# Optimization experiments

Hardware: AMD Instinct MI355X
Metric: run time of the kernel (lower is better)

## Reference

```python
import jax, jax.numpy as jnp
import numpy as np

N_QUBITS = 12
RANK = 1024
K = 4            # outcomes per qubit
D = 2 ** N_QUBITS
N_IDX = 1_000_000


def setup_inputs() -> dict:
    key = jax.random.key(0)
    k1, k2, k3, k4 = jax.random.split(key, 4)
    params = jax.random.normal(k1, (2, D, RANK), dtype=jnp.float32)
    M_real = jax.random.normal(k2, (K, 2, 2), dtype=jnp.float32)
    M_imag = jax.random.normal(k3, (K, 2, 2), dtype=jnp.float32)
    P_idxs = jax.random.randint(k4, (N_IDX,), 0, K ** N_QUBITS, dtype=jnp.int64)
    return {"params": params, "M_real": M_real, "M_imag": M_imag, "P_idxs": P_idxs}


def _qmt(rho, M, n_qubits):
    """Born rule: P[s1..sN] = Tr[(M_{s1} x ... x M_{sN}) rho].
    Sequential per-qubit contraction; T has shape [K^n, 2^(N-n), 2^(N-n)]."""
    T = rho[None, :, :]  # axes: (done outcomes, row legs j, col legs i)
    for _ in range(n_qubits):
        k, r, c = T.shape[0], T.shape[1] // 2, T.shape[2] // 2
        Tt = T.reshape(k, 2, r, 2, c)  # (k, j_n, j_rest, i_n, i_rest)
        # Tr contribution: sum_{i,j} M[s,i,j] * rho[j,i]
        T = jnp.einsum('sij,kjait->ksat', M, Tt).reshape(k * M.shape[0], r, c)
    return T.reshape(-1)  # [K^N] complex


def reference(params, M_real, M_imag, P_idxs):
    # rho = U U^H / Tr(U U^H)
    U = jax.lax.complex(params[0], params[1])            # [D, RANK] complex64
    rho = U @ U.conj().T                                  # [D, D]
    rho = rho / jnp.trace(rho)
    M = jax.lax.complex(M_real, M_imag)                   # [K, 2, 2] complex64
    P_all = _qmt(rho, M, N_QUBITS).real                   # [K^N] float32
    return P_all[P_idxs]
```

## Files before the change

### kernel.cpp

```cpp
#include <hip/hip_runtime.h>

#define D 4096
#define RANK 1024
#define UELEMS 4194304ULL
#define NTOT 16777216ULL
#define QSCALE 16000.0f

typedef __attribute__((ext_vector_type(4))) int i32x4;

__device__ float g_inv_tr[1];
__device__ float g_scale[D];
__device__ float g_mdre[16];
__device__ float g_mdim[16];

static __device__ __forceinline__ void load_lds16(const void* g, void* l) {
    __builtin_amdgcn_global_load_lds(
        (const __attribute__((address_space(1))) unsigned int*)g,
        (__attribute__((address_space(3))) unsigned int*)l, 16, 0, 0);
}

#define MFMA_I8 __builtin_amdgcn_mfma_i32_16x16x64_i8

__global__ __launch_bounds__(256) void convert_w_i8(const float* __restrict__ P,
                                                    const float* __restrict__ Mre,
                                                    const float* __restrict__ Mim,
                                                    char* __restrict__ Wh,
                                                    char* __restrict__ Wl)
{
    if (blockIdx.x == 0 && threadIdx.x < 16) {
        const int s = threadIdx.x >> 2, i = (threadIdx.x >> 1) & 1, j = threadIdx.x & 1;
        g_mdre[threadIdx.x] =  Mre[s * 4 + j * 2 + i];
        g_mdim[threadIdx.x] = -Mim[s * 4 + j * 2 + i];
    }

    const int w = threadIdx.x >> 6, lane = threadIdx.x & 63;
    const int row = blockIdx.x * 4 + w;

    float ur[16], ui[16];
    const float* pr = P + (size_t)row * RANK + lane * 16;
    const float* pi = P + UELEMS + (size_t)row * RANK + lane * 16;
    #pragma unroll
    for (int q = 0; q < 4; ++q) {
        const float4 a = ((const float4*)pr)[q];
        const float4 b = ((const float4*)pi)[q];
        ur[q * 4 + 0] = a.x; ur[q * 4 + 1] = a.y; ur[q * 4 + 2] = a.z; ur[q * 4 + 3] = a.w;
        ui[q * 4 + 0] = b.x; ui[q * 4 + 1] = b.y; ui[q * 4 + 2] = b.z; ui[q * 4 + 3] = b.w;
    }
    float mx = 0.f;
    #pragma unroll
    for (int e = 0; e < 16; ++e)
        mx = fmaxf(mx, fmaxf(fabsf(ur[e]), fabsf(ui[e])));
    #pragma unroll
    for (int off = 1; off < 64; off <<= 1)
        mx = fmaxf(mx, __shfl_xor(mx, off));
    const float inv = mx > 0.f ? QSCALE / mx : 0.f;
    if (lane == 0) g_scale[row] = mx / QSCALE;

    int hr[16], lr[16], hi[16], li[16];
    #pragma unroll
    for (int e = 0; e < 16; ++e) {
        float q = ur[e] * inv;
        float hf = rintf(q * 0.0078125f);
        hr[e] = (int)hf; lr[e] = (int)rintf(q - 128.f * hf);
        q = ui[e] * inv;
        hf = rintf(q * 0.0078125f);
        hi[e] = (int)hf; li[e] = (int)rintf(q - 128.f * hf);
    }
    uint4 phr, plr, phi, pli;
    unsigned* dst[4] = {(unsigned*)&phr, (unsigned*)&plr, (unsigned*)&phi, (unsigned*)&pli};
    #pragma unroll
    for (int q = 0; q < 4; ++q) {
        unsigned a = 0, b = 0, c = 0, d = 0;
        #pragma unroll
        for (int k = 0; k < 4; ++k) {
            const int sh = k * 8;
            a |= (unsigned)(hr[q * 4 + k] & 255) << sh;
            b |= (unsigned)(lr[q * 4 + k] & 255) << sh;
            c |= (unsigned)(hi[q * 4 + k] & 255) << sh;
            d |= (unsigned)(li[q * 4 + k] & 255) << sh;
        }
        dst[0][q] = a; dst[1][q] = b; dst[2][q] = c; dst[3][q] = d;
    }
    const size_t b1 = (size_t)row * 2048 + lane * 16;
    *(uint4*)&Wh[b1] = phr;          *(uint4*)&Wl[b1] = plr;
    *(uint4*)&Wh[b1 + 1024] = phi;   *(uint4*)&Wl[b1 + 1024] = pli;
}

__global__ __launch_bounds__(256, 2) void gemm_rho_i8(const char* __restrict__ Wh,
                                                      const char* __restrict__ Wl,
                                                      float2* __restrict__ rho)
{
    __shared__ __align__(16) char sA[2][4][64 * 64];
    __shared__ __align__(16) char sB[2][4][64 * 64];

    const int g = blockIdx.x;
    int bi = (int)((sqrtf(8.f * (float)g + 1.f) - 1.f) * 0.5f);
    while (bi * (bi + 1) / 2 > g) --bi;
    while ((bi + 1) * (bi + 2) / 2 <= g) ++bi;
    const int bj = g - bi * (bi + 1) / 2;
    const int row0 = bi << 6, col0 = bj << 6;

    const int t = threadIdx.x;
    const int lane = t & 63, w = t >> 6;
    const int wr = w >> 1, wc = w & 1;

    const int ra = t >> 2;
    const int kca = (t & 3) ^ ((ra >> 1) & 3);
    const size_t aoff = (size_t)(row0 + ra) * 2048 + kca * 16;
    const size_t boff = (size_t)(col0 + ra) * 2048 + kca * 16;
    const int ldso = t * 16;

    const int m = lane & 15, gq = lane >> 4;
    const int fko = (gq ^ ((m >> 1) & 3)) * 16;

    i32x4 rehh[2][2], remx[2][2], iphh[2][2], ipmx[2][2], iqhh[2][2], iqmx[2][2];
    #pragma unroll
    for (int i = 0; i < 2; ++i)
        #pragma unroll
        for (int j = 0; j < 2; ++j) {
            rehh[i][j] = (i32x4){0, 0, 0, 0}; remx[i][j] = (i32x4){0, 0, 0, 0};
            iphh[i][j] = (i32x4){0, 0, 0, 0}; ipmx[i][j] = (i32x4){0, 0, 0, 0};
            iqhh[i][j] = (i32x4){0, 0, 0, 0}; iqmx[i][j] = (i32x4){0, 0, 0, 0};
        }

    char* const sA0 = &sA[0][0][0];
    char* const sB0 = &sB[0][0][0];

    load_lds16(Wh + aoff,        sA0 + ldso);
    load_lds16(Wl + aoff,        sA0 + 4096  + ldso);
    load_lds16(Wh + aoff + 1024, sA0 + 8192  + ldso);
    load_lds16(Wl + aoff + 1024, sA0 + 12288 + ldso);
    load_lds16(Wh + boff,        sB0 + ldso);
    load_lds16(Wl + boff,        sB0 + 4096  + ldso);
    load_lds16(Wh + boff + 1024, sB0 + 8192  + ldso);
    load_lds16(Wl + boff + 1024, sB0 + 12288 + ldso);
    __syncthreads();

#define DO_MFMA_J(j)                                                          \
    _Pragma("unroll")                                                         \
    for (int i = 0; i < 2; ++i) {                                             \
        i32x4 r;                                                              \
        r = rehh[i][j];                                                       \
        r = MFMA_I8(fa1h[i], b1h[j], r, 0, 0, 0);                             \
        r = MFMA_I8(fa2h[i], b2h[j], r, 0, 0, 0);                             \
        rehh[i][j] = r;                                                       \
        r = remx[i][j];                                                       \
        r = MFMA_I8(fa1h[i], b1l[j], r, 0, 0, 0);                             \
        r = MFMA_I8(fa1l[i], b1h[j], r, 0, 0, 0);                             \
        r = MFMA_I8(fa2h[i], b2l[j], r, 0, 0, 0);                             \
        r = MFMA_I8(fa2l[i], b2h[j], r, 0, 0, 0);                             \
        remx[i][j] = r;                                                       \
        r = MFMA_I8(fa2h[i], b1h[j], iphh[i][j], 0, 0, 0); iphh[i][j] = r;    \
        r = ipmx[i][j];                                                       \
        r = MFMA_I8(fa2h[i], b1l[j], r, 0, 0, 0);                             \
        r = MFMA_I8(fa2l[i], b1h[j], r, 0, 0, 0);                             \
        ipmx[i][j] = r;                                                       \
        r = MFMA_I8(fa1h[i], b2h[j], iqhh[i][j], 0, 0, 0); iqhh[i][j] = r;    \
        r = iqmx[i][j];                                                       \
        r = MFMA_I8(fa1h[i], b2l[j], r, 0, 0, 0);                             \
        r = MFMA_I8(fa1l[i], b2h[j], r, 0, 0, 0);                             \
        iqmx[i][j] = r;                                                       \
    }

    #pragma unroll 2
    for (int kt = 0; kt < 16; ++kt) {
        const int cur = kt & 1;
        const char* sAc = sA0 + cur * 16384;
        const char* sBc = sB0 + cur * 16384;
        char* sAn = sA0 + (cur ^ 1) * 16384;
        char* sBn = sB0 + (cur ^ 1) * 16384;
        const size_t ko = (size_t)(kt + 1) * 64;

        if (kt < 15) {
            load_lds16(Wh + aoff + ko,        sAn + ldso);
            load_lds16(Wl + aoff + ko,        sAn + 4096  + ldso);
            load_lds16(Wh + aoff + ko + 1024, sAn + 8192  + ldso);
            load_lds16(Wl + aoff + ko + 1024, sAn + 12288 + ldso);
            load_lds16(Wh + boff + ko,        sBn + ldso);
            load_lds16(Wl + boff + ko,        sBn + 4096  + ldso);
            load_lds16(Wh + boff + ko + 1024, sBn + 8192  + ldso);
            load_lds16(Wl + boff + ko + 1024, sBn + 12288 + ldso);
        }

        i32x4 fa1h[2], fa1l[2], fa2h[2], fa2l[2];
        i32x4 b1h[2], b1l[2], b2h[2], b2l[2];
        #pragma unroll
        for (int i = 0; i < 2; ++i) {
            const int off = (wr * 32 + i * 16 + m) * 64 + fko;
            fa1h[i] = *(const i32x4*)(sAc + off);
            fa1l[i] = *(const i32x4*)(sAc + 4096  + off);
            fa2h[i] = *(const i32x4*)(sAc + 8192  + off);
            fa2l[i] = *(const i32x4*)(sAc + 12288 + off);
        }
        #pragma unroll
        for (int j = 0; j < 2; ++j) {
            const int off = (wc * 32 + j * 16 + m) * 64 + fko;
            b1h[j] = *(const i32x4*)(sBc + off);
            b1l[j] = *(const i32x4*)(sBc + 4096  + off);
            b2h[j] = *(const i32x4*)(sBc + 8192  + off);
            b2l[j] = *(const i32x4*)(sBc + 12288 + off);
        }

        __builtin_amdgcn_s_setprio(1);
        DO_MFMA_J(0)
        DO_MFMA_J(1)
        __builtin_amdgcn_s_setprio(0);

        __syncthreads();
    }
#undef DO_MFMA_J

    #pragma unroll
    for (int j = 0; j < 2; ++j) {
        const int col = col0 + wc * 32 + j * 16 + m;
        const float sc = g_scale[col];
        const int c64 = col >> 6;
        #pragma unroll
        for (int i = 0; i < 2; ++i) {
            #pragma unroll
            for (int r = 0; r < 4; ++r) {
                const int row = row0 + wr * 32 + i * 16 + gq * 4 + r;
                const float s2 = g_scale[row] * sc;
                const float re = s2 * (16384.f * (float)rehh[i][j][r] + 128.f * (float)remx[i][j][r]);
                const float im = s2 * (16384.f * (float)(iphh[i][j][r] - iqhh[i][j][r])
                                      + 128.f * (float)(ipmx[i][j][r] - iqmx[i][j][r]));
                const int r64 = row >> 6;
                if (r64 > c64 || row >= col) rho[(size_t)row * D + col] = make_float2(re, im);
                if (r64 == c64 && row > col) rho[(size_t)col * D + row] = make_float2(re, -im);
            }
        }
    }
}

__global__ void trace_inv(const float2* __restrict__ rho)
{
    __shared__ float red[256];
    float s = 0.f;
    for (int d = threadIdx.x; d < D; d += 256)
        s += rho[(size_t)d * (D + 1)].x;
    red[threadIdx.x] = s;
    __syncthreads();
    for (int off = 128; off > 0; off >>= 1) {
        if (threadIdx.x < off) red[threadIdx.x] += red[threadIdx.x + off];
        __syncthreads();
    }
    if (threadIdx.x == 0) g_inv_tr[0] = 1.0f / red[0];
}

static __device__ __forceinline__ void qmt2(float2* x,
                                            const float* __restrict__ Mre,
                                            const float* __restrict__ Mim)
{
    float2 y[16];
    #pragma unroll
    for (int sb = 0; sb < 4; ++sb)
        #pragma unroll
        for (int ja = 0; ja < 2; ++ja)
            #pragma unroll
            for (int ia = 0; ia < 2; ++ia) {
                float2 acc = make_float2(0.f, 0.f);
                #pragma unroll
                for (int ib = 0; ib < 2; ++ib)
                    #pragma unroll
                    for (int jb = 0; jb < 2; ++jb) {
                        const float mr = Mre[sb * 4 + ib * 2 + jb];
                        const float mi = Mim[sb * 4 + ib * 2 + jb];
                        const float2 v = x[(ja * 2 + jb) * 4 + ia * 2 + ib];
                        acc.x += mr * v.x - mi * v.y;
                        acc.y += mr * v.y + mi * v.x;
                    }
                y[sb * 4 + ja * 2 + ia] = acc;
            }
    #pragma unroll
    for (int sa = 0; sa < 4; ++sa)
        #pragma unroll
        for (int sb = 0; sb < 4; ++sb) {
            float2 acc = make_float2(0.f, 0.f);
            #pragma unroll
            for (int ia = 0; ia < 2; ++ia)
                #pragma unroll
                for (int ja = 0; ja < 2; ++ja) {
                    const float mr = Mre[sa * 4 + ia * 2 + ja];
                    const float mi = Mim[sa * 4 + ia * 2 + ja];
                    const float2 v = y[sb * 4 + ja * 2 + ia];
                    acc.x += mr * v.x - mi * v.y;
                    acc.y += mr * v.y + mi * v.x;
                }
            x[sa * 4 + sb] = acc;
        }
}

static __device__ __forceinline__ void pA_pipeline(float2* x, float2* X, const int t,
                                                   const float* __restrict__ mre,
                                                   const float* __restrict__ mim)
{
    qmt2(x, mre, mim);
    #pragma unroll
    for (int d = 0; d < 16; ++d) X[t * 17 + d] = x[d];
    __syncthreads();
    const int a2 = t >> 6, t2 = (t >> 4) & 3, d1 = t & 15;
    #pragma unroll
    for (int j2 = 0; j2 < 4; ++j2)
        #pragma unroll
        for (int i2 = 0; i2 < 4; ++i2)
            x[j2 * 4 + i2] = X[((a2 * 4 + j2) * 16 + t2 * 4 + i2) * 17 + d1];
    __syncthreads();
    qmt2(x, mre, mim);
    #pragma unroll
    for (int d = 0; d < 16; ++d) X[(a2 * 4 + t2) * 257 + d * 16 + d1] = x[d];
    __syncthreads();
    const int e2 = t >> 4, e1 = t & 15;
    #pragma unroll
    for (int j2 = 0; j2 < 4; ++j2)
        #pragma unroll
        for (int i2 = 0; i2 < 4; ++i2)
            x[j2 * 4 + i2] = X[(j2 * 4 + i2) * 257 + e2 * 16 + e1];
    qmt2(x, mre, mim);
}

__global__ __launch_bounds__(256) void qmt_pAh(const float2* __restrict__ in,
                                               float2* __restrict__ out,
                                               const float* __restrict__ Mre,
                                               const float* __restrict__ Mim)
{
    __shared__ __align__(16) float2 X[256 * 17];
    const int t = threadIdx.x;
    const int g = blockIdx.x;
    int rr = (int)((sqrtf(8.f * (float)g + 1.f) - 1.f) * 0.5f);
    while (rr * (rr + 1) / 2 > g) --rr;
    while ((rr + 1) * (rr + 2) / 2 <= g) ++rr;
    const int cc = g - rr * (rr + 1) / 2;

    const int a4 = t >> 4, t4 = t & 15;
    float2 x0[16], x[16];
    #pragma unroll
    for (int j2 = 0; j2 < 4; ++j2) {
        const float2* p = in + ((size_t)(rr * 64 + a4 * 4 + j2)) * 4096 + cc * 64 + t4 * 4;
        const float4 v0 = ((const float4*)p)[0];
        const float4 v1 = ((const float4*)p)[1];
        x0[j2 * 4 + 0] = make_float2(v0.x, v0.y);
        x0[j2 * 4 + 1] = make_float2(v0.z, v0.w);
        x0[j2 * 4 + 2] = make_float2(v1.x, v1.y);
        x0[j2 * 4 + 3] = make_float2(v1.z, v1.w);
    }

    #pragma unroll
    for (int q = 0; q < 16; ++q) x[q] = x0[q];
    pA_pipeline(x, X, t, Mre, Mim);
    const int e2 = t >> 4, e1 = t & 15;
    const size_t ob0 = (size_t)(rr * 64 + cc) * 4096 + e2 * 16 + e1;
    #pragma unroll
    for (int d = 0; d < 16; ++d) out[ob0 + (size_t)d * 256] = x[d];

    if (rr != cc) {
        __syncthreads();
        #pragma unroll
        for (int q = 0; q < 16; ++q) x[q] = x0[q];
        pA_pipeline(x, X, t, g_mdre, g_mdim);
        const size_t ob1 = (size_t)(cc * 64 + rr) * 4096 + e2 * 16 + e1;
        #pragma unroll
        for (int d = 0; d < 16; ++d)
            out[ob1 + (size_t)d * 256] = make_float2(x[d].x, -x[d].y);
    }
}

static __device__ __forceinline__ void qmt_stage_cb_half(float2* x,
                                                         const float* __restrict__ Mre,
                                                         const float* __restrict__ Mim)
{
    #pragma unroll
    for (int jb = 0; jb < 2; ++jb) {
        float2 y[16];
        #pragma unroll
        for (int sc = 0; sc < 4; ++sc)
            #pragma unroll
            for (int ii = 0; ii < 4; ++ii) {
                float2 acc = make_float2(0.f, 0.f);
                #pragma unroll
                for (int ic = 0; ic < 2; ++ic)
                    #pragma unroll
                    for (int jc = 0; jc < 2; ++jc) {
                        const float mr = Mre[sc * 4 + ic * 2 + jc];
                        const float mi = Mim[sc * 4 + ic * 2 + jc];
                        const float2 v = x[jb * 16 + jc * 8 + ii * 2 + ic];
                        acc.x += mr * v.x - mi * v.y;
                        acc.y += mr * v.y + mi * v.x;
                    }
                y[sc * 4 + ii] = acc;
            }
        #pragma unroll
        for (int q = 0; q < 16; ++q) x[jb * 16 + q] = y[q];
    }
    #pragma unroll
    for (int sc = 0; sc < 4; ++sc) {
        float2 z[8];
        #pragma unroll
        for (int sb = 0; sb < 4; ++sb)
            #pragma unroll
            for (int ia = 0; ia < 2; ++ia) {
                float2 acc = make_float2(0.f, 0.f);
                #pragma unroll
                for (int ib = 0; ib < 2; ++ib)
                    #pragma unroll
                    for (int jb = 0; jb < 2; ++jb) {
                        const float mr = Mre[sb * 4 + ib * 2 + jb];
                        const float mi = Mim[sb * 4 + ib * 2 + jb];
                        const float2 v = x[jb * 16 + sc * 4 + ia * 2 + ib];
                        acc.x += mr * v.x - mi * v.y;
                        acc.y += mr * v.y + mi * v.x;
                    }
                z[sb * 2 + ia] = acc;
            }
        #pragma unroll
        for (int sb = 0; sb < 4; ++sb)
            #pragma unroll
            for (int ia = 0; ia < 2; ++ia)
                x[(sb >> 1) * 16 + sc * 4 + ia * 2 + (sb & 1)] = z[sb * 2 + ia];
    }
}

#define STAGE_A_COEFFS                                                        \
    float Are[2][2], Aim[2][2], Bre[2][2], Bim[2][2];                         \
    _Pragma("unroll")                                                         \
    for (int sal = 0; sal < 2; ++sal)                                         \
        _Pragma("unroll")                                                     \
        for (int ia = 0; ia < 2; ++ia) {                                      \
            const int sa = 2 * h + sal;                                       \
            Are[sal][ia] = Mre[sa * 4 + ia * 2 + h];                          \
            Aim[sal][ia] = Mim[sa * 4 + ia * 2 + h];                          \
            Bre[sal][ia] = Mre[sa * 4 + ia * 2 + (1 - h)];                    \
            Bim[sal][ia] = Mim[sa * 4 + ia * 2 + (1 - h)];                    \
        }

__global__ __launch_bounds__(256) void qmt_p3(const float2* __restrict__ in,
                                              float2* __restrict__ out,
                                              const float* __restrict__ Mre,
                                              const float* __restrict__ Mim)
{
    const int t = threadIdx.x;
    const int h = (t >> 5) & 1;
    const int idx = blockIdx.x * 4 + (t >> 6);
    const int rc = idx >> 7;
    const int r3 = rc >> 3, c3 = rc & 7;
    const int s = (idx & 127) * 32 + (t & 31);

    float2 x[32];
    #pragma unroll
    for (int jb = 0; jb < 2; ++jb)
        #pragma unroll
        for (int jc = 0; jc < 2; ++jc) {
            const int j3 = 4 * h + 2 * jb + jc;
            #pragma unroll
            for (int i3 = 0; i3 < 8; ++i3)
                x[jb * 16 + jc * 8 + i3] =
                    in[(size_t)((r3 * 8 + j3) * 64 + c3 * 8 + i3) * 4096 + s];
        }

    qmt_stage_cb_half(x, Mre, Mim);

    STAGE_A_COEFFS
    const size_t ob = ((size_t)(r3 * 8 + c3) * 64) * 4096 + s;
    #pragma unroll
    for (int sbH = 0; sbH < 2; ++sbH)
        #pragma unroll
        for (int sc = 0; sc < 4; ++sc)
            #pragma unroll
            for (int sbL = 0; sbL < 2; ++sbL) {
                const int q = sbH * 16 + sc * 4 + sbL;
                const float2 o0 = x[q], o1 = x[q + 2];
                float2 r0, r1;
                r0.x = __shfl_xor(o0.x, 32); r0.y = __shfl_xor(o0.y, 32);
                r1.x = __shfl_xor(o1.x, 32); r1.y = __shfl_xor(o1.y, 32);
                const int sb = sbH * 2 + sbL;
                #pragma unroll
                for (int sal = 0; sal < 2; ++sal) {
                    const float re = Are[sal][0] * o0.x - Aim[sal][0] * o0.y
                                   + Are[sal][1] * o1.x - Aim[sal][1] * o1.y
                                   + Bre[sal][0] * r0.x - Bim[sal][0] * r0.y
                                   + Bre[sal][1] * r1.x - Bim[sal][1] * r1.y;
                    const float im = Are[sal][0] * o0.y + Aim[sal][0] * o0.x
                                   + Are[sal][1] * o1.y + Aim[sal][1] * o1.x
                                   + Bre[sal][0] * r0.y + Bim[sal][0] * r0.x
                                   + Bre[sal][1] * r1.y + Bim[sal][1] * r1.x;
                    const int s3 = (2 * h + sal) * 16 + sb * 4 + sc;
                    out[ob + (size_t)s3 * 4096] = make_float2(re, im);
                }
            }
}

__global__ __launch_bounds__(256) void qmt_p4(const float2* __restrict__ in,
                                              float* __restrict__ out,
                                              const float* __restrict__ Mre,
                                              const float* __restrict__ Mim)
{
    const int t = threadIdx.x;
    const int h = (t >> 5) & 1;
    const int s = (blockIdx.x * 4 + (t >> 6)) * 32 + (t & 31);

    float2 x[32];
    #pragma unroll
    for (int jb = 0; jb < 2; ++jb)
        #pragma unroll
        for (int jc = 0; jc < 2; ++jc) {
            const int j3 = 4 * h + 2 * jb + jc;
            #pragma unroll
            for (int i3 = 0; i3 < 8; ++i3)
                x[jb * 16 + jc * 8 + i3] = in[(size_t)(j3 * 8 + i3) * 262144 + s];
        }

    qmt_stage_cb_half(x, Mre, Mim);

    STAGE_A_COEFFS
    const size_t ob = (size_t)(s >> 5) * 2048 + (s & 31);
    #pragma unroll
    for (int sbH = 0; sbH < 2; ++sbH)
        #pragma unroll
        for (int sc = 0; sc < 4; ++sc)
            #pragma unroll
            for (int sbL = 0; sbL < 2; ++sbL) {
                const int q = sbH * 16 + sc * 4 + sbL;
                const float2 o0 = x[q], o1 = x[q + 2];
                float2 r0, r1;
                r0.x = __shfl_xor(o0.x, 32); r0.y = __shfl_xor(o0.y, 32);
                r1.x = __shfl_xor(o1.x, 32); r1.y = __shfl_xor(o1.y, 32);
                const int sb = sbH * 2 + sbL;
                #pragma unroll
                for (int sal = 0; sal < 2; ++sal) {
                    const float re = Are[sal][0] * o0.x - Aim[sal][0] * o0.y
                                   + Are[sal][1] * o1.x - Aim[sal][1] * o1.y
                                   + Bre[sal][0] * r0.x - Bim[sal][0] * r0.y
                                   + Bre[sal][1] * r1.x - Bim[sal][1] * r1.y;
                    const int s3 = (2 * h + sal) * 16 + sb * 4 + sc;
                    out[ob + (size_t)s3 * 32] = re;
                }
            }
}

__global__ void gather_idx(const float* __restrict__ P, const int* __restrict__ idxs,
                           float* __restrict__ out, const int n)
{
    const int i = blockIdx.x * 256 + threadIdx.x;
    if (i < n) {
        const int idx = idxs[i];
        const int s = idx & 262143;
        const size_t pos = (size_t)(s >> 5) * 2048 + (size_t)(idx >> 18) * 32 + (s & 31);
        out[i] = P[pos] * g_inv_tr[0];
    }
}

extern "C" void kernel_launch(void* const* d_in, const int* in_sizes, int n_in,
                              void* d_out, int out_size, void* d_ws, size_t ws_size,
                              hipStream_t stream)
{
    const float* params = (const float*)d_in[0];
    const float* Mre    = (const float*)d_in[1];
    const float* Mim    = (const float*)d_in[2];
    const int*   idxs   = (const int*)d_in[3];
    float*       out    = (float*)d_out;

    float* ws = (float*)d_ws;
    float2* A  = (float2*)ws;
    float2* Bp = (float2*)(ws + 2 * NTOT);
    char* Wh = (char*)Bp;
    char* Wl = Wh + (size_t)D * 2048;

    convert_w_i8<<<1024, 256, 0, stream>>>(params, Mre, Mim, Wh, Wl);
    gemm_rho_i8<<<2080, 256, 0, stream>>>(Wh, Wl, A);
    trace_inv<<<1, 256, 0, stream>>>(A);

    qmt_pAh<<<2080, 256, 0, stream>>>(A, Bp, Mre, Mim);
    qmt_p3<<<2048, 256, 0, stream>>>(Bp, A, Mre, Mim);
    qmt_p4<<<2048, 256, 0, stream>>>(A, (float*)Bp, Mre, Mim);

    gather_idx<<<(out_size + 255) / 256, 256, 0, stream>>>((float*)Bp, idxs, out, out_size);
}
```

Measured before the change: 388.5 us.

## Software-pipeline LDS fragment reads with MFMA and remap blocks across XCDs

Restructures the int8 rho GEMM main loop so register fragments for the next k-tile are read from LDS while the MFMAs for the current tile run, using two register fragment sets and ping-pong LDS buffers. It also remaps block IDs so consecutive blocks land on the same XCD group ((g0&7)*260 + g0>>3), aiming for better L2 reuse of shared rows and columns. The cost is doubled fragment registers, which may raise VGPR pressure under launch_bounds(256,2). The remap assumes the grid size is exactly 8*260 triangular tiles.

```diff
diff --git a/kernel.cpp b/kernel.cpp
--- a/kernel.cpp
+++ b/kernel.cpp
@@ -93,7 +93,9 @@
     __shared__ __align__(16) char sA[2][4][64 * 64];
     __shared__ __align__(16) char sB[2][4][64 * 64];
 
-    const int g = blockIdx.x;
+    const int g0 = blockIdx.x;
+    const int g = (g0 & 7) * 260 + (g0 >> 3);
+
     int bi = (int)((sqrtf(8.f * (float)g + 1.f) - 1.f) * 0.5f);
     while (bi * (bi + 1) / 2 > g) --bi;
     while ((bi + 1) * (bi + 2) / 2 <= g) ++bi;
@@ -126,89 +128,101 @@
     char* const sA0 = &sA[0][0][0];
     char* const sB0 = &sB[0][0][0];
 
-    load_lds16(Wh + aoff,        sA0 + ldso);
-    load_lds16(Wl + aoff,        sA0 + 4096  + ldso);
-    load_lds16(Wh + aoff + 1024, sA0 + 8192  + ldso);
-    load_lds16(Wl + aoff + 1024, sA0 + 12288 + ldso);
-    load_lds16(Wh + boff,        sB0 + ldso);
-    load_lds16(Wl + boff,        sB0 + 4096  + ldso);
-    load_lds16(Wh + boff + 1024, sB0 + 8192  + ldso);
-    load_lds16(Wl + boff + 1024, sB0 + 12288 + ldso);
+#define STAGE(bn, kt)                                                         \
+    {                                                                         \
+        const size_t ko_ = (size_t)(kt) * 64;                                 \
+        char* dA_ = sA0 + (bn) * 16384;                                       \
+        char* dB_ = sB0 + (bn) * 16384;                                       \
+        load_lds16(Wh + aoff + ko_,        dA_ + ldso);                       \
+        load_lds16(Wl + aoff + ko_,        dA_ + 4096  + ldso);               \
+        load_lds16(Wh + aoff + ko_ + 1024, dA_ + 8192  + ldso);               \
+        load_lds16(Wl + aoff + ko_ + 1024, dA_ + 12288 + ldso);               \
+        load_lds16(Wh + boff + ko_,        dB_ + ldso);                       \
+        load_lds16(Wl + boff + ko_,        dB_ + 4096  + ldso);               \
+        load_lds16(Wh + boff + ko_ + 1024, dB_ + 8192  + ldso);               \
+        load_lds16(Wl + boff + ko_ + 1024, dB_ + 12288 + ldso);               \
+    }
+
+#define READ_FRAGS(P, bn)                                                     \
+    {                                                                         \
+        const char* rA_ = sA0 + (bn) * 16384;                                 \
+        const char* rB_ = sB0 + (bn) * 16384;                                 \
+        _Pragma("unroll")                                                     \
+        for (int i = 0; i < 2; ++i) {                                         \
+            const int off = (wr * 32 + i * 16 + m) * 64 + fko;                \
+            P##a1h[i] = *(const i32x4*)(rA_ + off);                          \
+            P##a1l[i] = *(const i32x4*)(rA_ + 4096  + off);                  \
+            P##a2h[i] = *(const i32x4*)(rA_ + 8192  + off);                  \
+            P##a2l[i] = *(const i32x4*)(rA_ + 12288 + off);                  \
+        }                                                                     \
+        _Pragma("unroll")                                                     \
+        for (int j = 0; j < 2; ++j) {                                         \
+            const int off = (wc * 32 + j * 16 + m) * 64 + fko;                \
+            P##b1h[j] = *(const i32x4*)(rB_ + off);                          \
+            P##b1l[j] = *(const i32x4*)(rB_ + 4096  + off);                  \
+            P##b2h[j] = *(const i32x4*)(rB_ + 8192  + off);                  \
+            P##b2l[j] = *(const i32x4*)(rB_ + 12288 + off);                  \
+        }                                                                     \
+    }
+
+#define DO_MFMA(P)                                                            \
+    _Pragma("unroll")                                                         \
+    for (int j = 0; j < 2; ++j)                                               \
+        _Pragma("unroll")                                                     \
+        for (int i = 0; i < 2; ++i) {                                         \
+            i32x4 r;                                                          \
+            r = rehh[i][j];                                                   \
+            r = MFMA_I8(P##a1h[i], P##b1h[j], r, 0, 0, 0);                    \
+            r = MFMA_I8(P##a2h[i], P##b2h[j], r, 0, 0, 0);                    \
+            rehh[i][j] = r;                                                   \
+            r = remx[i][j];                                                   \
+            r = MFMA_I8(P##a1h[i], P##b1l[j], r, 0, 0, 0);                    \
+            r = MFMA_I8(P##a1l[i], P##b1h[j], r, 0, 0, 0);                    \
+            r = MFMA_I8(P##a2h[i], P##b2l[j], r, 0, 0, 0);                    \
+            r = MFMA_I8(P##a2l[i], P##b2h[j], r, 0, 0, 0);                    \
+            remx[i][j] = r;                                                   \
+            r = MFMA_I8(P##a2h[i], P##b1h[j], iphh[i][j], 0, 0, 0);           \
+            iphh[i][j] = r;                                                   \
+            r = ipmx[i][j];                                                   \
+            r = MFMA_I8(P##a2h[i], P##b1l[j], r, 0, 0, 0);                    \
+            r = MFMA_I8(P##a2l[i], P##b1h[j], r, 0, 0, 0);                    \
+            ipmx[i][j] = r;                                                   \
+            r = MFMA_I8(P##a1h[i], P##b2h[j], iqhh[i][j], 0, 0, 0);           \
+            iqhh[i][j] = r;                                                   \
+            r = iqmx[i][j];                                                   \
+            r = MFMA_I8(P##a1h[i], P##b2l[j], r, 0, 0, 0);                    \
+            r = MFMA_I8(P##a1l[i], P##b2h[j], r, 0, 0, 0);                    \
+            iqmx[i][j] = r;                                                   \
+        }
+
+    i32x4 Aa1h[2], Aa1l[2], Aa2h[2], Aa2l[2], Ab1h[2], Ab1l[2], Ab2h[2], Ab2l[2];
+    i32x4 Ba1h[2], Ba1l[2], Ba2h[2], Ba2l[2], Bb1h[2], Bb1l[2], Bb2h[2], Bb2l[2];
+
+    STAGE(0, 0)
     __syncthreads();
-
-#define DO_MFMA_J(j)                                                          \
-    _Pragma("unroll")                                                         \
-    for (int i = 0; i < 2; ++i) {                                             \
-        i32x4 r;                                                              \
-        r = rehh[i][j];                                                       \
-        r = MFMA_I8(fa1h[i], b1h[j], r, 0, 0, 0);                             \
-        r = MFMA_I8(fa2h[i], b2h[j], r, 0, 0, 0);                             \
-        rehh[i][j] = r;                                                       \
-        r = remx[i][j];                                                       \
-        r = MFMA_I8(fa1h[i], b1l[j], r, 0, 0, 0);                             \
-        r = MFMA_I8(fa1l[i], b1h[j], r, 0, 0, 0);                             \
-        r = MFMA_I8(fa2h[i], b2l[j], r, 0, 0, 0);                             \
-        r = MFMA_I8(fa2l[i], b2h[j], r, 0, 0, 0);                             \
-        remx[i][j] = r;                                                       \
-        r = MFMA_I8(fa2h[i], b1h[j], iphh[i][j], 0, 0, 0); iphh[i][j] = r;    \
-        r = ipmx[i][j];                                                       \
-        r = MFMA_I8(fa2h[i], b1l[j], r, 0, 0, 0);                             \
-        r = MFMA_I8(fa2l[i], b1h[j], r, 0, 0, 0);                             \
-        ipmx[i][j] = r;                                                       \
-        r = MFMA_I8(fa1h[i], b2h[j], iqhh[i][j], 0, 0, 0); iqhh[i][j] = r;    \
-        r = iqmx[i][j];                                                       \
-        r = MFMA_I8(fa1h[i], b2l[j], r, 0, 0, 0);                             \
-        r = MFMA_I8(fa1l[i], b2h[j], r, 0, 0, 0);                             \
-        iqmx[i][j] = r;                                                       \
-    }
-
-    #pragma unroll 2
-    for (int kt = 0; kt < 16; ++kt) {
-        const int cur = kt & 1;
-        const char* sAc = sA0 + cur * 16384;
-        const char* sBc = sB0 + cur * 16384;
-        char* sAn = sA0 + (cur ^ 1) * 16384;
-        char* sBn = sB0 + (cur ^ 1) * 16384;
-        const size_t ko = (size_t)(kt + 1) * 64;
-
-        if (kt < 15) {
-            load_lds16(Wh + aoff + ko,        sAn + ldso);
-            load_lds16(Wl + aoff + ko,        sAn + 4096  + ldso);
-            load_lds16(Wh + aoff + ko + 1024, sAn + 8192  + ldso);
-            load_lds16(Wl + aoff + ko + 1024, sAn + 12288 + ldso);
-            load_lds16(Wh + boff + ko,        sBn + ldso);
-            load_lds16(Wl + boff + ko,        sBn + 4096  + ldso);
-            load_lds16(Wh + boff + ko + 1024, sBn + 8192  + ldso);
-            load_lds16(Wl + boff + ko + 1024, sBn + 12288 + ldso);
-        }
-
-        i32x4 fa1h[2], fa1l[2], fa2h[2], fa2l[2];
-        i32x4 b1h[2], b1l[2], b2h[2], b2l[2];
-        #pragma unroll
-        for (int i = 0; i < 2; ++i) {
-            const int off = (wr * 32 + i * 16 + m) * 64 + fko;
-            fa1h[i] = *(const i32x4*)(sAc + off);
-            fa1l[i] = *(const i32x4*)(sAc + 4096  + off);
-            fa2h[i] = *(const i32x4*)(sAc + 8192  + off);
-            fa2l[i] = *(const i32x4*)(sAc + 12288 + off);
-        }
-        #pragma unroll
-        for (int j = 0; j < 2; ++j) {
-            const int off = (wc * 32 + j * 16 + m) * 64 + fko;
-            b1h[j] = *(const i32x4*)(sBc + off);
-            b1l[j] = *(const i32x4*)(sBc + 4096  + off);
-            b2h[j] = *(const i32x4*)(sBc + 8192  + off);
-            b2l[j] = *(const i32x4*)(sBc + 12288 + off);
-        }
-
+    READ_FRAGS(A, 0)
+    STAGE(1, 1)
+
+    for (int it = 0; it < 8; ++it) {
+        __syncthreads();
+        if (it < 7) STAGE(0, 2 * it + 2)
+        READ_FRAGS(B, 1)
         __builtin_amdgcn_s_setprio(1);
-        DO_MFMA_J(0)
-        DO_MFMA_J(1)
+        DO_MFMA(A)
         __builtin_amdgcn_s_setprio(0);
 
         __syncthreads();
-    }
-#undef DO_MFMA_J
+        if (it < 7) {
+            STAGE(1, 2 * it + 3)
+            READ_FRAGS(A, 0)
+        }
+        __builtin_amdgcn_s_setprio(1);
+        DO_MFMA(B)
+        __builtin_amdgcn_s_setprio(0);
+    }
+#undef STAGE
+#undef READ_FRAGS
+#undef DO_MFMA
 
     #pragma unroll
     for (int j = 0; j < 2; ++j) {
```

Result: slower. 468.8 us (+20.7%).

## Load B operand directly from a fragment-ordered global copy, bypassing LDS

Applied to the files above, without the earlier changes.

The conversion kernel now also writes a second int8 copy of the hi/lo real/imag planes, laid out in MFMA-fragment order by k-chunk and row. The Gram GEMM reads its B fragments straight from global memory into registers, which drops the B LDS buffers and halves the shared-memory staging traffic. Block indices are also permuted with an 8-way stride to change the order in which tiles are scheduled, with cache reuse in mind. The cost is an extra 16 MB write in the convert kernel, and the B loads are no longer prefetched a stage ahead, so their global latency may stall the MFMA loop.

```diff
diff --git a/kernel.cpp b/kernel.cpp
--- a/kernel.cpp
+++ b/kernel.cpp
@@ -25,7 +25,8 @@
                                                     const float* __restrict__ Mre,
                                                     const float* __restrict__ Mim,
                                                     char* __restrict__ Wh,
-                                                    char* __restrict__ Wl)
+                                                    char* __restrict__ Wl,
+                                                    char* __restrict__ W2)
 {
     if (blockIdx.x == 0 && threadIdx.x < 16) {
         const int s = threadIdx.x >> 2, i = (threadIdx.x >> 1) & 1, j = threadIdx.x & 1;
@@ -84,16 +85,24 @@
     const size_t b1 = (size_t)row * 2048 + lane * 16;
     *(uint4*)&Wh[b1] = phr;          *(uint4*)&Wl[b1] = plr;
     *(uint4*)&Wh[b1 + 1024] = phi;   *(uint4*)&Wl[b1 + 1024] = pli;
+
+    const size_t b2 = ((size_t)lane * 4096 + row) * 16;
+    *(uint4*)&W2[b2]                = phr;
+    *(uint4*)&W2[b2 + 4194304]      = plr;
+    *(uint4*)&W2[b2 + 8388608]      = phi;
+    *(uint4*)&W2[b2 + 12582912]     = pli;
 }
 
 __global__ __launch_bounds__(256, 2) void gemm_rho_i8(const char* __restrict__ Wh,
                                                       const char* __restrict__ Wl,
+                                                      const char* __restrict__ W2,
                                                       float2* __restrict__ rho)
 {
     __shared__ __align__(16) char sA[2][4][64 * 64];
-    __shared__ __align__(16) char sB[2][4][64 * 64];
-
-    const int g = blockIdx.x;
+
+    const int g0 = blockIdx.x;
+    const int g = (g0 & 7) * 260 + (g0 >> 3);
+
     int bi = (int)((sqrtf(8.f * (float)g + 1.f) - 1.f) * 0.5f);
     while (bi * (bi + 1) / 2 > g) --bi;
     while ((bi + 1) * (bi + 2) / 2 <= g) ++bi;
@@ -107,11 +116,12 @@
     const int ra = t >> 2;
     const int kca = (t & 3) ^ ((ra >> 1) & 3);
     const size_t aoff = (size_t)(row0 + ra) * 2048 + kca * 16;
-    const size_t boff = (size_t)(col0 + ra) * 2048 + kca * 16;
     const int ldso = t * 16;
 
     const int m = lane & 15, gq = lane >> 4;
     const int fko = (gq ^ ((m >> 1) & 3)) * 16;
+
+    const size_t bcol = ((size_t)gq * 4096 + col0 + wc * 32 + m) * 16;
 
     i32x4 rehh[2][2], remx[2][2], iphh[2][2], ipmx[2][2], iqhh[2][2], iqmx[2][2];
     #pragma unroll
@@ -124,66 +134,40 @@
         }
 
     char* const sA0 = &sA[0][0][0];
-    char* const sB0 = &sB[0][0][0];
-
-    load_lds16(Wh + aoff,        sA0 + ldso);
-    load_lds16(Wl + aoff,        sA0 + 4096  + ldso);
-    load_lds16(Wh + aoff + 1024, sA0 + 8192  + ldso);
-    load_lds16(Wl + aoff + 1024, sA0 + 12288 + ldso);
-    load_lds16(Wh + boff,        sB0 + ldso);
-    load_lds16(Wl + boff,        sB0 + 4096  + ldso);
-    load_lds16(Wh + boff + 1024, sB0 + 8192  + ldso);
-    load_lds16(Wl + boff + 1024, sB0 + 12288 + ldso);
+
+#define STAGE_A(bn, kt)                                                       \
+    {                                                                         \
+        const size_t ko_ = (size_t)(kt) * 64;                                 \
+        char* dA_ = sA0 + (bn) * 16384;                                       \
+        load_lds16(Wh + aoff + ko_,        dA_ + ldso);                       \
+        load_lds16(Wl + aoff + ko_,        dA_ + 4096  + ldso);               \
+        load_lds16(Wh + aoff + ko_ + 1024, dA_ + 8192  + ldso);               \
+        load_lds16(Wl + aoff + ko_ + 1024, dA_ + 12288 + ldso);               \
+    }
+
+    STAGE_A(0, 0)
     __syncthreads();
-
-#define DO_MFMA_J(j)                                                          \
-    _Pragma("unroll")                                                         \
-    for (int i = 0; i < 2; ++i) {                                             \
-        i32x4 r;                                                              \
-        r = rehh[i][j];                                                       \
-        r = MFMA_I8(fa1h[i], b1h[j], r, 0, 0, 0);                             \
-        r = MFMA_I8(fa2h[i], b2h[j], r, 0, 0, 0);                             \
-        rehh[i][j] = r;                                                       \
-        r = remx[i][j];                                                       \
-        r = MFMA_I8(fa1h[i], b1l[j], r, 0, 0, 0);                             \
-        r = MFMA_I8(fa1l[i], b1h[j], r, 0, 0, 0);                             \
-        r = MFMA_I8(fa2h[i], b2l[j], r, 0, 0, 0);                             \
-        r = MFMA_I8(fa2l[i], b2h[j], r, 0, 0, 0);                             \
-        remx[i][j] = r;                                                       \
-        r = MFMA_I8(fa2h[i], b1h[j], iphh[i][j], 0, 0, 0); iphh[i][j] = r;    \
-        r = ipmx[i][j];                                                       \
-        r = MFMA_I8(fa2h[i], b1l[j], r, 0, 0, 0);                             \
-        r = MFMA_I8(fa2l[i], b1h[j], r, 0, 0, 0);                             \
-        ipmx[i][j] = r;                                                       \
-        r = MFMA_I8(fa1h[i], b2h[j], iqhh[i][j], 0, 0, 0); iqhh[i][j] = r;    \
-        r = iqmx[i][j];                                                       \
-        r = MFMA_I8(fa1h[i], b2l[j], r, 0, 0, 0);                             \
-        r = MFMA_I8(fa1l[i], b2h[j], r, 0, 0, 0);                             \
-        iqmx[i][j] = r;                                                       \
-    }
 
     #pragma unroll 2
     for (int kt = 0; kt < 16; ++kt) {
         const int cur = kt & 1;
         const char* sAc = sA0 + cur * 16384;
-        const char* sBc = sB0 + cur * 16384;
-        char* sAn = sA0 + (cur ^ 1) * 16384;
-        char* sBn = sB0 + (cur ^ 1) * 16384;
-        const size_t ko = (size_t)(kt + 1) * 64;
-
-        if (kt < 15) {
-            load_lds16(Wh + aoff + ko,        sAn + ldso);
-            load_lds16(Wl + aoff + ko,        sAn + 4096  + ldso);
-            load_lds16(Wh + aoff + ko + 1024, sAn + 8192  + ldso);
-            load_lds16(Wl + aoff + ko + 1024, sAn + 12288 + ldso);
-            load_lds16(Wh + boff + ko,        sBn + ldso);
-            load_lds16(Wl + boff + ko,        sBn + 4096  + ldso);
-            load_lds16(Wh + boff + ko + 1024, sBn + 8192  + ldso);
-            load_lds16(Wl + boff + ko + 1024, sBn + 12288 + ldso);
-        }
+
+        i32x4 b1h[2], b1l[2], b2h[2], b2l[2];
+        {
+            const char* pB = W2 + bcol + (size_t)kt * 262144;
+            #pragma unroll
+            for (int j = 0; j < 2; ++j) {
+                b1h[j] = *(const i32x4*)(pB + j * 256);
+                b1l[j] = *(const i32x4*)(pB + 4194304  + j * 256);
+                b2h[j] = *(const i32x4*)(pB + 8388608  + j * 256);
+                b2l[j] = *(const i32x4*)(pB + 12582912 + j * 256);
+            }
+        }
+
+        if (kt < 15) STAGE_A(cur ^ 1, kt + 1)
 
         i32x4 fa1h[2], fa1l[2], fa2h[2], fa2l[2];
-        i32x4 b1h[2], b1l[2], b2h[2], b2l[2];
         #pragma unroll
         for (int i = 0; i < 2; ++i) {
             const int off = (wr * 32 + i * 16 + m) * 64 + fko;
@@ -192,23 +176,41 @@
             fa2h[i] = *(const i32x4*)(sAc + 8192  + off);
             fa2l[i] = *(const i32x4*)(sAc + 12288 + off);
         }
-        #pragma unroll
-        for (int j = 0; j < 2; ++j) {
-            const int off = (wc * 32 + j * 16 + m) * 64 + fko;
-            b1h[j] = *(const i32x4*)(sBc + off);
-            b1l[j] = *(const i32x4*)(sBc + 4096  + off);
-            b2h[j] = *(const i32x4*)(sBc + 8192  + off);
-            b2l[j] = *(const i32x4*)(sBc + 12288 + off);
-        }
 
         __builtin_amdgcn_s_setprio(1);
-        DO_MFMA_J(0)
-        DO_MFMA_J(1)
+        #pragma unroll
+        for (int j = 0; j < 2; ++j)
+            #pragma unroll
+            for (int i = 0; i < 2; ++i) {
+                i32x4 r;
+                r = rehh[i][j];
+                r = MFMA_I8(fa1h[i], b1h[j], r, 0, 0, 0);
+                r = MFMA_I8(fa2h[i], b2h[j], r, 0, 0, 0);
+                rehh[i][j] = r;
+                r = remx[i][j];
+                r = MFMA_I8(fa1h[i], b1l[j], r, 0, 0, 0);
+                r = MFMA_I8(fa1l[i], b1h[j], r, 0, 0, 0);
+                r = MFMA_I8(fa2h[i], b2l[j], r, 0, 0, 0);
+                r = MFMA_I8(fa2l[i], b2h[j], r, 0, 0, 0);
+                remx[i][j] = r;
+                r = MFMA_I8(fa2h[i], b1h[j], iphh[i][j], 0, 0, 0);
+                iphh[i][j] = r;
+                r = ipmx[i][j];
+                r = MFMA_I8(fa2h[i], b1l[j], r, 0, 0, 0);
+                r = MFMA_I8(fa2l[i], b1h[j], r, 0, 0, 0);
+                ipmx[i][j] = r;
+                r = MFMA_I8(fa1h[i], b2h[j], iqhh[i][j], 0, 0, 0);
+                iqhh[i][j] = r;
+                r = iqmx[i][j];
+                r = MFMA_I8(fa1h[i], b2l[j], r, 0, 0, 0);
+                r = MFMA_I8(fa1l[i], b2h[j], r, 0, 0, 0);
+                iqmx[i][j] = r;
+            }
         __builtin_amdgcn_s_setprio(0);
 
         __syncthreads();
     }
-#undef DO_MFMA_J
+#undef STAGE_A
 
     #pragma unroll
     for (int j = 0; j < 2; ++j) {
@@ -563,9 +565,10 @@
     float2* Bp = (float2*)(ws + 2 * NTOT);
     char* Wh = (char*)Bp;
     char* Wl = Wh + (size_t)D * 2048;
-
-    convert_w_i8<<<1024, 256, 0, stream>>>(params, Mre, Mim, Wh, Wl);
-    gemm_rho_i8<<<2080, 256, 0, stream>>>(Wh, Wl, A);
+    char* W2 = Wl + (size_t)D * 2048;
+
+    convert_w_i8<<<1024, 256, 0, stream>>>(params, Mre, Mim, Wh, Wl, W2);
+    gemm_rho_i8<<<2080, 256, 0, stream>>>(Wh, Wl, W2, A);
     trace_inv<<<1, 256, 0, stream>>>(A);
 
     qmt_pAh<<<2080, 256, 0, stream>>>(A, Bp, Mre, Mim);
```

New measurement: 412.4 us. 6.2% more time.
